# Optimization experiments

Measured on AMD Instinct MI355X. Metric: run time of the kernel, lower is better.

The kernel has to match this reference:

```python
import jax, jax.numpy as jnp
import numpy as np
import math

INPUT_SIZE = 512
HIDDEN_SIZE = 1024
B, T = 64, 512


def setup_inputs() -> dict:
    key = jax.random.key(0)
    ks = jax.random.split(key, 8)
    stdv = 1.0 / math.sqrt(HIDDEN_SIZE)
    def U(k, shape):
        return jax.random.uniform(k, shape, jnp.float32, -stdv, stdv)
    x = jax.random.normal(ks[0], (B, T, INPUT_SIZE), jnp.float32)
    W_i_r = U(ks[1], (HIDDEN_SIZE, INPUT_SIZE))
    W_h_r = U(ks[2], (HIDDEN_SIZE, HIDDEN_SIZE))
    W_i_z = U(ks[3], (HIDDEN_SIZE, INPUT_SIZE))
    W_h_z = U(ks[4], (HIDDEN_SIZE, HIDDEN_SIZE))
    W_i_n = U(ks[5], (HIDDEN_SIZE, INPUT_SIZE))
    W_h_n = U(ks[6], (HIDDEN_SIZE, HIDDEN_SIZE))
    zeros = jnp.zeros((HIDDEN_SIZE,), jnp.float32)
    return {
        "x": x,
        "W_i_r": W_i_r, "b_i_r": zeros, "W_h_r": W_h_r, "b_h_r": zeros,
        "W_i_z": W_i_z, "b_i_z": zeros, "W_h_z": W_h_z, "b_h_z": zeros,
        "W_i_n": W_i_n, "b_i_n": zeros, "W_h_n": W_h_n, "b_h_n": zeros,
    }


def reference(x, W_i_r, b_i_r, W_h_r, b_h_r, W_i_z, b_i_z, W_h_z, b_h_z,
              W_i_n, b_i_n, W_h_n, b_h_n):
    Bn, Tn, _ = x.shape
    # Precompute all input projections in one batched matmul each: [B,T,H]
    xr = jnp.einsum('bti,hi->bth', x, W_i_r) + b_i_r
    xz = jnp.einsum('bti,hi->bth', x, W_i_z) + b_i_z
    xn = jnp.einsum('bti,hi->bth', x, W_i_n) + b_i_n

    h0 = jnp.zeros((Bn, W_h_r.shape[0]), x.dtype)

    def step(h, inp):
        xr_t, xz_t, xn_t = inp  # each [B,H]
        r = jax.nn.sigmoid(xr_t + h @ W_h_r.T + b_h_r)
        z = jax.nn.sigmoid(xz_t + h @ W_h_z.T + b_h_z)
        n = jnp.tanh(xn_t + r * (h @ W_h_n.T + b_h_n))
        h_new = (1.0 - z) * n + z * h
        return h_new, h_new

    # scan over time: inputs transposed to [T,B,H]
    xs = (xr.transpose(1, 0, 2), xz.transpose(1, 0, 2), xn.transpose(1, 0, 2))
    _, h_seq = jax.lax.scan(step, h0, xs)
    return h_seq.transpose(1, 0, 2)  # [B,T,H]
```

## Files before the change

kernel.cpp:

```cpp
#include <hip/hip_runtime.h>
#include <math.h>


#define BB 64
#define TT 512
#define II 512
#define HH 1024
#define JB 4
#define CK 128
#define PAD 132

__device__ __forceinline__ void fma4(float4& a, const float4 xv, const float4 w) {
    a.x += xv.x * w.x;
    a.y += xv.y * w.y;
    a.z += xv.z * w.z;
    a.w += xv.w * w.w;
}

__device__ __forceinline__ void accum_chunk(
    const float* __restrict__ xsrow,
    const float* __restrict__ wr, const float* __restrict__ wz,
    const float* __restrict__ wn,
    float4& aR, float4& aZ, float4& aN)
{
#pragma unroll
    for (int k4 = 0; k4 < CK / 4; ++k4) {
        float4 xv = *(const float4*)(xsrow + k4 * 4);
        fma4(aR, xv, *(const float4*)(wr + k4 * 4));
        fma4(aZ, xv, *(const float4*)(wz + k4 * 4));
        fma4(aN, xv, *(const float4*)(wn + k4 * 4));
    }
}

__global__ __launch_bounds__(256) void gru_step(
    const float* __restrict__ x,
    const float* __restrict__ Wir, const float* __restrict__ Whr,
    const float* __restrict__ Wiz, const float* __restrict__ Whz,
    const float* __restrict__ Win, const float* __restrict__ Whn,
    const float* __restrict__ bir, const float* __restrict__ bhr,
    const float* __restrict__ biz, const float* __restrict__ bhz,
    const float* __restrict__ bin_, const float* __restrict__ bhn,
    float* __restrict__ out, int t)
{
    __shared__ float xs[BB][PAD];
    const int tid = threadIdx.x;
    const int b   = tid & 63;
    const int jg  = tid >> 6;
    const int j   = __builtin_amdgcn_readfirstlane((int)blockIdx.x * JB + jg);

    float4 aR  = {0.f, 0.f, 0.f, 0.f};
    float4 aZ  = {0.f, 0.f, 0.f, 0.f};
    float4 aXN = {0.f, 0.f, 0.f, 0.f};
    float4 aHN = {0.f, 0.f, 0.f, 0.f};

    const float* xbase = x + (size_t)t * II;
    for (int kc = 0; kc < II / CK; ++kc) {
#pragma unroll
        for (int i = 0; i < 8; ++i) {
            int f   = tid + 256 * i;
            int row = f >> 5;
            int c4  = f & 31;
            *(float4*)&xs[row][c4 * 4] =
                *(const float4*)(xbase + (size_t)row * (TT * II) + kc * CK + c4 * 4);
        }
        __syncthreads();
        accum_chunk(&xs[b][0],
                    Wir + (size_t)j * II + kc * CK,
                    Wiz + (size_t)j * II + kc * CK,
                    Win + (size_t)j * II + kc * CK,
                    aR, aZ, aXN);
        __syncthreads();
    }

    if (t > 0) {
        const float* hbase = out + (size_t)(t - 1) * HH;
        for (int kc = 0; kc < HH / CK; ++kc) {
#pragma unroll
            for (int i = 0; i < 8; ++i) {
                int f   = tid + 256 * i;
                int row = f >> 5;
                int c4  = f & 31;
                *(float4*)&xs[row][c4 * 4] =
                    *(const float4*)(hbase + (size_t)row * (TT * HH) + kc * CK + c4 * 4);
            }
            __syncthreads();
            accum_chunk(&xs[b][0],
                        Whr + (size_t)j * HH + kc * CK,
                        Whz + (size_t)j * HH + kc * CK,
                        Whn + (size_t)j * HH + kc * CK,
                        aR, aZ, aHN);
            __syncthreads();
        }
    }

    float rpre = (aR.x + aR.y + aR.z + aR.w) + bir[j] + bhr[j];
    float zpre = (aZ.x + aZ.y + aZ.z + aZ.w) + biz[j] + bhz[j];
    float hn   = (aHN.x + aHN.y + aHN.z + aHN.w) + bhn[j];
    float xn   = (aXN.x + aXN.y + aXN.z + aXN.w) + bin_[j];

    float r = 1.f / (1.f + __expf(-rpre));
    float z = 1.f / (1.f + __expf(-zpre));
    float n = tanhf(xn + r * hn);

    float hprev = (t > 0) ? out[(size_t)b * (TT * HH) + (size_t)(t - 1) * HH + j] : 0.f;
    float hnew  = (1.f - z) * n + z * hprev;
    out[(size_t)b * (TT * HH) + (size_t)t * HH + j] = hnew;
}

extern "C" void kernel_launch(void* const* d_in, const int* in_sizes, int n_in,
                              void* d_out, int out_size, void* d_ws, size_t ws_size,
                              hipStream_t stream) {
    (void)in_sizes; (void)n_in; (void)d_ws; (void)ws_size; (void)out_size;

    const float* x    = (const float*)d_in[0];
    const float* Wir  = (const float*)d_in[1];
    const float* bir  = (const float*)d_in[2];
    const float* Whr  = (const float*)d_in[3];
    const float* bhr  = (const float*)d_in[4];
    const float* Wiz  = (const float*)d_in[5];
    const float* biz  = (const float*)d_in[6];
    const float* Whz  = (const float*)d_in[7];
    const float* bhz  = (const float*)d_in[8];
    const float* Win  = (const float*)d_in[9];
    const float* bin_ = (const float*)d_in[10];
    const float* Whn  = (const float*)d_in[11];
    const float* bhn  = (const float*)d_in[12];
    float* out = (float*)d_out;

    for (int t = 0; t < TT; ++t) {
        gru_step<<<dim3(HH / JB), dim3(256), 0, stream>>>(
            x, Wir, Whr, Wiz, Whz, Win, Whn,
            bir, bhr, biz, bhz, bin_, bhn, out, t);
    }
}
```

Measured before the change: 14.13 ms.

## Replace per-timestep launches with persistent cooperative kernel and grid sync

Fuses the 512 per-timestep kernel launches into one persistent cooperative kernel of 256 blocks that loops over time and uses grid.sync between steps. It also double-buffers the shared-memory staging, prefetching the next chunk into registers while the current one is computed, which removes one block barrier per chunk. Biases are hoisted out of the time loop. This removes launch overhead and per-step pipeline drain, at the cost of a grid-wide barrier each step and a dependence on all blocks being co-resident.

```diff
diff --git a/kernel.cpp b/kernel.cpp
--- a/kernel.cpp
+++ b/kernel.cpp
@@ -1,5 +1,8 @@
 #include <hip/hip_runtime.h>
+#include <hip/hip_cooperative_groups.h>
 #include <math.h>
+
+namespace cg = cooperative_groups;
 
 
 #define BB 64
@@ -32,7 +35,20 @@
     }
 }
 
-__global__ __launch_bounds__(256) void gru_step(
+__device__ __forceinline__ void issue_chunk(
+    float4 (&st)[8], const float* __restrict__ base, size_t rowstride,
+    int koff, int tid)
+{
+#pragma unroll
+    for (int i = 0; i < 8; ++i) {
+        int f   = tid + 256 * i;
+        int row = f >> 5;
+        int c4  = f & 31;
+        st[i] = *(const float4*)(base + (size_t)row * rowstride + koff + c4 * 4);
+    }
+}
+
+__global__ __launch_bounds__(256, 1) void gru_persistent(
     const float* __restrict__ x,
     const float* __restrict__ Wir, const float* __restrict__ Whr,
     const float* __restrict__ Wiz, const float* __restrict__ Whz,
@@ -40,71 +56,80 @@
     const float* __restrict__ bir, const float* __restrict__ bhr,
     const float* __restrict__ biz, const float* __restrict__ bhz,
     const float* __restrict__ bin_, const float* __restrict__ bhn,
-    float* __restrict__ out, int t)
+    float* __restrict__ out)
 {
-    __shared__ float xs[BB][PAD];
+    __shared__ float xs[2][BB][PAD];
+    cg::grid_group grid = cg::this_grid();
+
     const int tid = threadIdx.x;
     const int b   = tid & 63;
     const int jg  = tid >> 6;
     const int j   = __builtin_amdgcn_readfirstlane((int)blockIdx.x * JB + jg);
 
-    float4 aR  = {0.f, 0.f, 0.f, 0.f};
-    float4 aZ  = {0.f, 0.f, 0.f, 0.f};
-    float4 aXN = {0.f, 0.f, 0.f, 0.f};
-    float4 aHN = {0.f, 0.f, 0.f, 0.f};
+    const float bir_j = bir[j], bhr_j = bhr[j];
+    const float biz_j = biz[j], bhz_j = bhz[j];
+    const float bin_j = bin_[j], bhn_j = bhn[j];
 
-    const float* xbase = x + (size_t)t * II;
-    for (int kc = 0; kc < II / CK; ++kc) {
-#pragma unroll
-        for (int i = 0; i < 8; ++i) {
-            int f   = tid + 256 * i;
-            int row = f >> 5;
-            int c4  = f & 31;
-            *(float4*)&xs[row][c4 * 4] =
-                *(const float4*)(xbase + (size_t)row * (TT * II) + kc * CK + c4 * 4);
-        }
-        __syncthreads();
-        accum_chunk(&xs[b][0],
-                    Wir + (size_t)j * II + kc * CK,
-                    Wiz + (size_t)j * II + kc * CK,
-                    Win + (size_t)j * II + kc * CK,
-                    aR, aZ, aXN);
-        __syncthreads();
-    }
+    float4 st[8];
+    issue_chunk(st, x, (size_t)TT * II, 0, tid);
 
-    if (t > 0) {
+    for (int t = 0; t < TT; ++t) {
+        float4 aR  = {0.f, 0.f, 0.f, 0.f};
+        float4 aZ  = {0.f, 0.f, 0.f, 0.f};
+        float4 aXN = {0.f, 0.f, 0.f, 0.f};
+        float4 aHN = {0.f, 0.f, 0.f, 0.f};
+
+        const float* xbase = x   + (size_t)t * II;
         const float* hbase = out + (size_t)(t - 1) * HH;
-        for (int kc = 0; kc < HH / CK; ++kc) {
+        const int nch = (t > 0) ? 12 : 4;
+
+        for (int c = 0; c < nch; ++c) {
+            const int bufi = c & 1;
 #pragma unroll
             for (int i = 0; i < 8; ++i) {
-                int f   = tid + 256 * i;
-                int row = f >> 5;
-                int c4  = f & 31;
-                *(float4*)&xs[row][c4 * 4] =
-                    *(const float4*)(hbase + (size_t)row * (TT * HH) + kc * CK + c4 * 4);
+                const int f = tid + 256 * i;
+                *(float4*)&xs[bufi][f >> 5][(f & 31) * 4] = st[i];
             }
             __syncthreads();
-            accum_chunk(&xs[b][0],
-                        Whr + (size_t)j * HH + kc * CK,
-                        Whz + (size_t)j * HH + kc * CK,
-                        Whn + (size_t)j * HH + kc * CK,
-                        aR, aZ, aHN);
-            __syncthreads();
+            if (c + 1 < nch) {
+                if (c + 1 < 4)
+                    issue_chunk(st, xbase, (size_t)TT * II, (c + 1) * CK, tid);
+                else
+                    issue_chunk(st, hbase, (size_t)TT * HH, (c + 1 - 4) * CK, tid);
+            }
+            if (c < 4) {
+                accum_chunk(&xs[bufi][b][0],
+                            Wir + (size_t)j * II + c * CK,
+                            Wiz + (size_t)j * II + c * CK,
+                            Win + (size_t)j * II + c * CK,
+                            aR, aZ, aXN);
+            } else {
+                const int kc = c - 4;
+                accum_chunk(&xs[bufi][b][0],
+                            Whr + (size_t)j * HH + kc * CK,
+                            Whz + (size_t)j * HH + kc * CK,
+                            Whn + (size_t)j * HH + kc * CK,
+                            aR, aZ, aHN);
+            }
         }
+
+        float rpre = (aR.x + aR.y + aR.z + aR.w) + bir_j + bhr_j;
+        float zpre = (aZ.x + aZ.y + aZ.z + aZ.w) + biz_j + bhz_j;
+        float hn   = (aHN.x + aHN.y + aHN.z + aHN.w) + bhn_j;
+        float xn   = (aXN.x + aXN.y + aXN.z + aXN.w) + bin_j;
+
+        float r = 1.f / (1.f + __expf(-rpre));
+        float z = 1.f / (1.f + __expf(-zpre));
+        float n = tanhf(xn + r * hn);
+
+        float hprev = (t > 0) ? out[(size_t)b * (TT * HH) + (size_t)(t - 1) * HH + j] : 0.f;
+        out[(size_t)b * (TT * HH) + (size_t)t * HH + j] = (1.f - z) * n + z * hprev;
+
+        if (t + 1 < TT)
+            issue_chunk(st, xbase + II, (size_t)TT * II, 0, tid);
+
+        grid.sync();
     }
-
-    float rpre = (aR.x + aR.y + aR.z + aR.w) + bir[j] + bhr[j];
-    float zpre = (aZ.x + aZ.y + aZ.z + aZ.w) + biz[j] + bhz[j];
-    float hn   = (aHN.x + aHN.y + aHN.z + aHN.w) + bhn[j];
-    float xn   = (aXN.x + aXN.y + aXN.z + aXN.w) + bin_[j];
-
-    float r = 1.f / (1.f + __expf(-rpre));
-    float z = 1.f / (1.f + __expf(-zpre));
-    float n = tanhf(xn + r * hn);
-
-    float hprev = (t > 0) ? out[(size_t)b * (TT * HH) + (size_t)(t - 1) * HH + j] : 0.f;
-    float hnew  = (1.f - z) * n + z * hprev;
-    out[(size_t)b * (TT * HH) + (size_t)t * HH + j] = hnew;
 }
 
 extern "C" void kernel_launch(void* const* d_in, const int* in_sizes, int n_in,
@@ -127,9 +152,9 @@
     const float* bhn  = (const float*)d_in[12];
     float* out = (float*)d_out;
 
-    for (int t = 0; t < TT; ++t) {
-        gru_step<<<dim3(HH / JB), dim3(256), 0, stream>>>(
-            x, Wir, Whr, Wiz, Whz, Win, Whn,
-            bir, bhr, biz, bhz, bin_, bhn, out, t);
-    }
+    void* args[] = { &x, &Wir, &Whr, &Wiz, &Whz, &Win, &Whn,
+                     &bir, &bhr, &biz, &bhz, &bin_, &bhn, &out };
+
+    hipLaunchCooperativeKernel((const void*)gru_persistent,
+                               dim3(HH / JB), dim3(256), args, 0, stream);
 }
```

Measured after the change: 51.26 ms. 3.63x slower.

## Split K across two wavegroups and read hidden state from packed workspace

Applied to the files above, without the earlier changes.

Doubles the block to 512 threads so two halves of each block split the reduction dimension, then combine partial sums through shared memory. The hidden-state matmul now reads h directly from a double-buffered, interleaved workspace copy (laid out k4-major across batch) instead of staging strided rows of the output through LDS with barriers. This aims to cut per-step latency and barrier count on the serial time loop. It adds an extra reduction barrier and a second global write of h per step, and depends on the workspace being large enough.

```diff
diff --git a/kernel.cpp b/kernel.cpp
--- a/kernel.cpp
+++ b/kernel.cpp
@@ -7,7 +7,8 @@
 #define II 512
 #define HH 1024
 #define JB 4
-#define CK 128
+#define KHX 256
+#define KHH 512
 #define PAD 132
 
 __device__ __forceinline__ void fma4(float4& a, const float4 xv, const float4 w) {
@@ -17,22 +18,7 @@
     a.w += xv.w * w.w;
 }
 
-__device__ __forceinline__ void accum_chunk(
-    const float* __restrict__ xsrow,
-    const float* __restrict__ wr, const float* __restrict__ wz,
-    const float* __restrict__ wn,
-    float4& aR, float4& aZ, float4& aN)
-{
-#pragma unroll
-    for (int k4 = 0; k4 < CK / 4; ++k4) {
-        float4 xv = *(const float4*)(xsrow + k4 * 4);
-        fma4(aR, xv, *(const float4*)(wr + k4 * 4));
-        fma4(aZ, xv, *(const float4*)(wz + k4 * 4));
-        fma4(aN, xv, *(const float4*)(wn + k4 * 4));
-    }
-}
-
-__global__ __launch_bounds__(256) void gru_step(
+__global__ __launch_bounds__(512, 2) void gru_step(
     const float* __restrict__ x,
     const float* __restrict__ Wir, const float* __restrict__ Whr,
     const float* __restrict__ Wiz, const float* __restrict__ Whz,
@@ -40,13 +26,19 @@
     const float* __restrict__ bir, const float* __restrict__ bhr,
     const float* __restrict__ biz, const float* __restrict__ bhz,
     const float* __restrict__ bin_, const float* __restrict__ bhn,
-    float* __restrict__ out, int t)
+    float* __restrict__ out, float* __restrict__ htpack, int t)
 {
-    __shared__ float xs[BB][PAD];
-    const int tid = threadIdx.x;
-    const int b   = tid & 63;
-    const int jg  = tid >> 6;
-    const int j   = __builtin_amdgcn_readfirstlane((int)blockIdx.x * JB + jg);
+    __shared__ float xs[2][BB][PAD];
+    const int tid  = threadIdx.x;
+    const int b    = tid & 63;
+    const int sel  = tid >> 6;
+    const int jloc = sel & 3;
+    const int kh   = sel >> 2;
+    const int j    = __builtin_amdgcn_readfirstlane((int)blockIdx.x * JB + jloc);
+
+    const float bir_j = bir[j], bhr_j = bhr[j];
+    const float biz_j = biz[j], bhz_j = bhz[j];
+    const float bin_j = bin_[j], bhn_j = bhn[j];
 
     float4 aR  = {0.f, 0.f, 0.f, 0.f};
     float4 aZ  = {0.f, 0.f, 0.f, 0.f};
@@ -54,63 +46,89 @@
     float4 aHN = {0.f, 0.f, 0.f, 0.f};
 
     const float* xbase = x + (size_t)t * II;
-    for (int kc = 0; kc < II / CK; ++kc) {
+    for (int p = 0; p < 2; ++p) {
 #pragma unroll
         for (int i = 0; i < 8; ++i) {
-            int f   = tid + 256 * i;
-            int row = f >> 5;
-            int c4  = f & 31;
-            *(float4*)&xs[row][c4 * 4] =
-                *(const float4*)(xbase + (size_t)row * (TT * II) + kc * CK + c4 * 4);
+            int f    = tid + 512 * i;
+            int vrow = f >> 5;
+            int c4   = f & 31;
+            int row  = vrow & 63;
+            int half = vrow >> 6;
+            int koff = half * KHX + p * 128;
+            *(float4*)&xs[half][row][c4 * 4] =
+                *(const float4*)(xbase + (size_t)row * (TT * II) + koff + c4 * 4);
         }
         __syncthreads();
-        accum_chunk(&xs[b][0],
-                    Wir + (size_t)j * II + kc * CK,
-                    Wiz + (size_t)j * II + kc * CK,
-                    Win + (size_t)j * II + kc * CK,
-                    aR, aZ, aXN);
+        {
+            const float* xsrow = &xs[kh][b][0];
+            const int kw = kh * KHX + p * 128;
+            const float* wr = Wir + (size_t)j * II + kw;
+            const float* wz = Wiz + (size_t)j * II + kw;
+            const float* wn = Win + (size_t)j * II + kw;
+#pragma unroll
+            for (int k4 = 0; k4 < 32; ++k4) {
+                float4 xv = *(const float4*)(xsrow + k4 * 4);
+                fma4(aR,  xv, *(const float4*)(wr + k4 * 4));
+                fma4(aZ,  xv, *(const float4*)(wz + k4 * 4));
+                fma4(aXN, xv, *(const float4*)(wn + k4 * 4));
+            }
+        }
         __syncthreads();
     }
 
     if (t > 0) {
-        const float* hbase = out + (size_t)(t - 1) * HH;
-        for (int kc = 0; kc < HH / CK; ++kc) {
-#pragma unroll
-            for (int i = 0; i < 8; ++i) {
-                int f   = tid + 256 * i;
-                int row = f >> 5;
-                int c4  = f & 31;
-                *(float4*)&xs[row][c4 * 4] =
-                    *(const float4*)(hbase + (size_t)row * (TT * HH) + kc * CK + c4 * 4);
-            }
-            __syncthreads();
-            accum_chunk(&xs[b][0],
-                        Whr + (size_t)j * HH + kc * CK,
-                        Whz + (size_t)j * HH + kc * CK,
-                        Whn + (size_t)j * HH + kc * CK,
-                        aR, aZ, aHN);
-            __syncthreads();
+        const float* hp = htpack + (size_t)((t - 1) & 1) * (HH * BB);
+        const int kbase = kh * KHH;
+        const float* hrow = hp + (size_t)(kbase >> 2) * (BB * 4) + b * 4;
+        const float* wr = Whr + (size_t)j * HH + kbase;
+        const float* wz = Whz + (size_t)j * HH + kbase;
+        const float* wn = Whn + (size_t)j * HH + kbase;
+#pragma unroll 4
+        for (int k4 = 0; k4 < KHH / 4; ++k4) {
+            float4 hv = *(const float4*)(hrow + (size_t)k4 * (BB * 4));
+            fma4(aR,  hv, *(const float4*)(wr + k4 * 4));
+            fma4(aZ,  hv, *(const float4*)(wz + k4 * 4));
+            fma4(aHN, hv, *(const float4*)(wn + k4 * 4));
         }
     }
 
-    float rpre = (aR.x + aR.y + aR.z + aR.w) + bir[j] + bhr[j];
-    float zpre = (aZ.x + aZ.y + aZ.z + aZ.w) + biz[j] + bhz[j];
-    float hn   = (aHN.x + aHN.y + aHN.z + aHN.w) + bhn[j];
-    float xn   = (aXN.x + aXN.y + aXN.z + aXN.w) + bin_[j];
+    __syncthreads();
+    float* red = &xs[0][0][0];
+    if (kh == 1) {
+        float* r4 = red + ((jloc * 64 + b) * 4);
+        r4[0] = aR.x + aR.y + aR.z + aR.w;
+        r4[1] = aZ.x + aZ.y + aZ.z + aZ.w;
+        r4[2] = aXN.x + aXN.y + aXN.z + aXN.w;
+        r4[3] = aHN.x + aHN.y + aHN.z + aHN.w;
+    }
+    __syncthreads();
+    if (kh == 0) {
+        const float* r4 = red + ((jloc * 64 + b) * 4);
+        float rpre = (aR.x + aR.y + aR.z + aR.w) + r4[0] + bir_j + bhr_j;
+        float zpre = (aZ.x + aZ.y + aZ.z + aZ.w) + r4[1] + biz_j + bhz_j;
+        float xn   = (aXN.x + aXN.y + aXN.z + aXN.w) + r4[2] + bin_j;
+        float hn   = (aHN.x + aHN.y + aHN.z + aHN.w) + r4[3] + bhn_j;
 
-    float r = 1.f / (1.f + __expf(-rpre));
-    float z = 1.f / (1.f + __expf(-zpre));
-    float n = tanhf(xn + r * hn);
+        float r = 1.f / (1.f + __expf(-rpre));
+        float z = 1.f / (1.f + __expf(-zpre));
+        float n = tanhf(xn + r * hn);
 
-    float hprev = (t > 0) ? out[(size_t)b * (TT * HH) + (size_t)(t - 1) * HH + j] : 0.f;
-    float hnew  = (1.f - z) * n + z * hprev;
-    out[(size_t)b * (TT * HH) + (size_t)t * HH + j] = hnew;
+        float hprev = 0.f;
+        if (t > 0)
+            hprev = htpack[(size_t)((t - 1) & 1) * (HH * BB)
+                           + (size_t)(j >> 2) * (BB * 4) + b * 4 + (j & 3)];
+        float hnew = (1.f - z) * n + z * hprev;
+
+        out[(size_t)b * (TT * HH) + (size_t)t * HH + j] = hnew;
+        htpack[(size_t)(t & 1) * (HH * BB)
+               + (size_t)(j >> 2) * (BB * 4) + b * 4 + (j & 3)] = hnew;
+    }
 }
 
 extern "C" void kernel_launch(void* const* d_in, const int* in_sizes, int n_in,
                               void* d_out, int out_size, void* d_ws, size_t ws_size,
                               hipStream_t stream) {
-    (void)in_sizes; (void)n_in; (void)d_ws; (void)ws_size; (void)out_size;
+    (void)in_sizes; (void)n_in; (void)ws_size; (void)out_size;
 
     const float* x    = (const float*)d_in[0];
     const float* Wir  = (const float*)d_in[1];
@@ -125,11 +143,12 @@
     const float* bin_ = (const float*)d_in[10];
     const float* Whn  = (const float*)d_in[11];
     const float* bhn  = (const float*)d_in[12];
-    float* out = (float*)d_out;
+    float* out    = (float*)d_out;
+    float* htpack = (float*)d_ws;
 
     for (int t = 0; t < TT; ++t) {
-        gru_step<<<dim3(HH / JB), dim3(256), 0, stream>>>(
+        gru_step<<<dim3(HH / JB), dim3(512), 0, stream>>>(
             x, Wir, Whr, Wiz, Whz, Win, Whn,
-            bir, bhr, biz, bhz, bin_, bhn, out, t);
+            bir, bhr, biz, bhz, bin_, bhn, out, htpack, t);
     }
 }
```

Result: slower. 29.30 ms (+107.4%).

## Hoist input projections into one batched kernel before the recurrent loop

Applied to the files above, without the earlier changes.

Adds an xproj kernel that computes all three input-gate projections for every timestep in a single highly parallel launch and stores them in workspace. The per-step kernel then reads these precomputed values and does only the hidden-state matvecs. This takes the input projection off the serial critical path. In exchange it needs a large workspace buffer of 3*T*H*B floats and keeps the old path as a fallback when the workspace is too small.

```diff
diff --git a/kernel.cpp b/kernel.cpp
--- a/kernel.cpp
+++ b/kernel.cpp
@@ -9,6 +9,7 @@
 #define JB 4
 #define CK 128
 #define PAD 132
+#define XJ 16
 
 __device__ __forceinline__ void fma4(float4& a, const float4 xv, const float4 w) {
     a.x += xv.x * w.x;
@@ -17,6 +18,132 @@
     a.w += xv.w * w.w;
 }
 
+__global__ __launch_bounds__(256) void xproj(
+    const float* __restrict__ x,
+    const float* __restrict__ Wir, const float* __restrict__ Wiz,
+    const float* __restrict__ Win, float* __restrict__ xpre)
+{
+    __shared__ float xs[BB][PAD];
+    const int tid  = threadIdx.x;
+    const int b    = tid & 63;
+    const int w    = tid >> 6;
+    const int bid  = (int)blockIdx.x;
+    const int t    = bid >> 6;
+    const int jgrp = bid & 63;
+    const int j0   = __builtin_amdgcn_readfirstlane(jgrp * XJ + w * 4);
+
+    float4 acc[4][3];
+#pragma unroll
+    for (int jj = 0; jj < 4; ++jj)
+#pragma unroll
+        for (int g = 0; g < 3; ++g)
+            acc[jj][g] = {0.f, 0.f, 0.f, 0.f};
+
+    const float* xbase = x + (size_t)t * II;
+    for (int kc = 0; kc < II / CK; ++kc) {
+#pragma unroll
+        for (int i = 0; i < 8; ++i) {
+            int f   = tid + 256 * i;
+            int row = f >> 5;
+            int c4  = f & 31;
+            *(float4*)&xs[row][c4 * 4] =
+                *(const float4*)(xbase + (size_t)row * (TT * II) + kc * CK + c4 * 4);
+        }
+        __syncthreads();
+        const float* xsrow = &xs[b][0];
+#pragma unroll
+        for (int k4 = 0; k4 < CK / 4; ++k4) {
+            float4 xv = *(const float4*)(xsrow + k4 * 4);
+#pragma unroll
+            for (int jj = 0; jj < 4; ++jj) {
+                const size_t wof = (size_t)(j0 + jj) * II + kc * CK + k4 * 4;
+                fma4(acc[jj][0], xv, *(const float4*)(Wir + wof));
+                fma4(acc[jj][1], xv, *(const float4*)(Wiz + wof));
+                fma4(acc[jj][2], xv, *(const float4*)(Win + wof));
+            }
+        }
+        __syncthreads();
+    }
+
+#pragma unroll
+    for (int jj = 0; jj < 4; ++jj) {
+        const int j = j0 + jj;
+#pragma unroll
+        for (int g = 0; g < 3; ++g) {
+            float s = acc[jj][g].x + acc[jj][g].y + acc[jj][g].z + acc[jj][g].w;
+            xpre[(((size_t)g * TT + t) * HH + j) * BB + b] = s;
+        }
+    }
+}
+
+__global__ __launch_bounds__(256) void gru_step_h(
+    const float* __restrict__ Whr, const float* __restrict__ Whz,
+    const float* __restrict__ Whn,
+    const float* __restrict__ bir, const float* __restrict__ bhr,
+    const float* __restrict__ biz, const float* __restrict__ bhz,
+    const float* __restrict__ bin_, const float* __restrict__ bhn,
+    const float* __restrict__ xpre,
+    float* __restrict__ out, int t)
+{
+    __shared__ float xs[BB][PAD];
+    const int tid = threadIdx.x;
+    const int b   = tid & 63;
+    const int jg  = tid >> 6;
+    const int j   = __builtin_amdgcn_readfirstlane((int)blockIdx.x * JB + jg);
+
+    const float bir_j = bir[j], bhr_j = bhr[j];
+    const float biz_j = biz[j], bhz_j = bhz[j];
+    const float bin_j = bin_[j], bhn_j = bhn[j];
+    const float xr  = xpre[(((size_t)0 * TT + t) * HH + j) * BB + b];
+    const float xz  = xpre[(((size_t)1 * TT + t) * HH + j) * BB + b];
+    const float xn0 = xpre[(((size_t)2 * TT + t) * HH + j) * BB + b];
+    float hprev = 0.f;
+    if (t > 0)
+        hprev = out[(size_t)b * (TT * HH) + (size_t)(t - 1) * HH + j];
+
+    float4 aR  = {0.f, 0.f, 0.f, 0.f};
+    float4 aZ  = {0.f, 0.f, 0.f, 0.f};
+    float4 aHN = {0.f, 0.f, 0.f, 0.f};
+
+    if (t > 0) {
+        const float* hbase = out + (size_t)(t - 1) * HH;
+        for (int kc = 0; kc < HH / CK; ++kc) {
+#pragma unroll
+            for (int i = 0; i < 8; ++i) {
+                int f   = tid + 256 * i;
+                int row = f >> 5;
+                int c4  = f & 31;
+                *(float4*)&xs[row][c4 * 4] =
+                    *(const float4*)(hbase + (size_t)row * (TT * HH) + kc * CK + c4 * 4);
+            }
+            __syncthreads();
+            const float* xsrow = &xs[b][0];
+            const float* wr = Whr + (size_t)j * HH + kc * CK;
+            const float* wz = Whz + (size_t)j * HH + kc * CK;
+            const float* wn = Whn + (size_t)j * HH + kc * CK;
+#pragma unroll
+            for (int k4 = 0; k4 < CK / 4; ++k4) {
+                float4 xv = *(const float4*)(xsrow + k4 * 4);
+                fma4(aR,  xv, *(const float4*)(wr + k4 * 4));
+                fma4(aZ,  xv, *(const float4*)(wz + k4 * 4));
+                fma4(aHN, xv, *(const float4*)(wn + k4 * 4));
+            }
+            __syncthreads();
+        }
+    }
+
+    float rpre = (aR.x + aR.y + aR.z + aR.w) + xr + bir_j + bhr_j;
+    float zpre = (aZ.x + aZ.y + aZ.z + aZ.w) + xz + biz_j + bhz_j;
+    float hn   = (aHN.x + aHN.y + aHN.z + aHN.w) + bhn_j;
+    float xn   = xn0 + bin_j;
+
+    float r = 1.f / (1.f + __expf(-rpre));
+    float z = 1.f / (1.f + __expf(-zpre));
+    float n = tanhf(xn + r * hn);
+
+    out[(size_t)b * (TT * HH) + (size_t)t * HH + j] = (1.f - z) * n + z * hprev;
+}
+
 __device__ __forceinline__ void accum_chunk(
     const float* __restrict__ xsrow,
     const float* __restrict__ wr, const float* __restrict__ wz,
@@ -32,7 +159,7 @@
     }
 }
 
-__global__ __launch_bounds__(256) void gru_step(
+__global__ __launch_bounds__(256) void gru_step_full(
     const float* __restrict__ x,
     const float* __restrict__ Wir, const float* __restrict__ Whr,
     const float* __restrict__ Wiz, const float* __restrict__ Whz,
@@ -103,14 +230,13 @@
     float n = tanhf(xn + r * hn);
 
     float hprev = (t > 0) ? out[(size_t)b * (TT * HH) + (size_t)(t - 1) * HH + j] : 0.f;
-    float hnew  = (1.f - z) * n + z * hprev;
-    out[(size_t)b * (TT * HH) + (size_t)t * HH + j] = hnew;
+    out[(size_t)b * (TT * HH) + (size_t)t * HH + j] = (1.f - z) * n + z * hprev;
 }
 
 extern "C" void kernel_launch(void* const* d_in, const int* in_sizes, int n_in,
                               void* d_out, int out_size, void* d_ws, size_t ws_size,
                               hipStream_t stream) {
-    (void)in_sizes; (void)n_in; (void)d_ws; (void)ws_size; (void)out_size;
+    (void)in_sizes; (void)n_in; (void)out_size;
 
     const float* x    = (const float*)d_in[0];
     const float* Wir  = (const float*)d_in[1];
@@ -127,9 +253,19 @@
     const float* bhn  = (const float*)d_in[12];
     float* out = (float*)d_out;
 
-    for (int t = 0; t < TT; ++t) {
-        gru_step<<<dim3(HH / JB), dim3(256), 0, stream>>>(
-            x, Wir, Whr, Wiz, Whz, Win, Whn,
-            bir, bhr, biz, bhz, bin_, bhn, out, t);
-    }
-}
+    const size_t need = (size_t)3 * TT * HH * BB * sizeof(float);
+    if (d_ws != nullptr && ws_size >= need) {
+        float* xpre = (float*)d_ws;
+        xproj<<<dim3(TT * 64), dim3(256), 0, stream>>>(x, Wir, Wiz, Win, xpre);
+        for (int t = 0; t < TT; ++t) {
+            gru_step_h<<<dim3(HH / JB), dim3(256), 0, stream>>>(
+                Whr, Whz, Whn, bir, bhr, biz, bhz, bin_, bhn, xpre, out, t);
+        }
+    } else {
+        for (int t = 0; t < TT; ++t) {
+            gru_step_full<<<dim3(HH / JB), dim3(256), 0, stream>>>(
+                x, Wir, Whr, Wiz, Whz, Win, Whn,
+                bir, bhr, biz, bhz, bin_, bhn, out, t);
+        }
+    }
+}
```

Result: slower. 15.86 ms (+12.3%).
